# Optimization experiments

Measured on AMD Instinct MI355X. Metric: run time of the kernel, lower is better.

Reference implementation:

```python
import jax, jax.numpy as jnp
import numpy as np

STALK_DIM = 8
K = 5
MARGIN = 0.5
TAU = 0.01
EPS_GAP = 1e-4


def _sheaf_eigenvalues(points, W):
    """Eigenvalues of the sheaf Laplacian L = delta^T delta on a point cloud.

    points: (n, d_in), W: (s, d_in) projection weight (nn.Linear, no bias).
    Faithful to the torch loop, but assembles L directly from its s x s blocks
    (L = delta^T delta expanded per edge) instead of materializing dense delta.
    """
    X = points @ W.T                       # (n, s)
    n, s = X.shape

    # --- fixed topology: KNN on detached coordinates (torch no_grad) ---
    Xd = jax.lax.stop_gradient(X)
    d2 = jnp.sum((Xd[:, None, :] - Xd[None, :, :]) ** 2, axis=-1)  # (n, n)
    nn_idx = jnp.argsort(d2, axis=1)[:, 1:K + 1]                    # (n, K), skip self
    A = jnp.zeros((n, n), dtype=bool).at[jnp.arange(n)[:, None], nn_idx].set(True)
    A = A | A.T                                                     # undirected
    triu = jnp.triu(jnp.ones((n, n), dtype=bool), 1)
    M = (A & triu).astype(points.dtype)    # (n, n) edge mask, canonical i < j

    # --- restriction maps for all ordered pairs i < j (mask selects edges) ---
    d = X[None, :, :] - X[:, None, :]      # d[i, j] = X[j] - X[i], (n, n, s)
    dn = jnp.linalg.norm(d, axis=-1) + 1e-12
    dhat = d / dn[..., None]
    alpha = jnp.minimum(dn, 1.0)
    I_s = jnp.eye(s, dtype=points.dtype)
    # R_ij = I - alpha * dhat dhat^T   (n, n, s, s)
    R = I_s - alpha[..., None, None] * (dhat[..., :, None] * dhat[..., None, :])
    RtR = jnp.einsum('ijab,ijac->ijbc', R, R)

    # --- L = delta^T delta, per edge (i<j): row block [.. I .. -R ..]
    #     contributes  L[i,i]+=I,  L[j,j]+=R^T R,  L[i,j]+=-R,  L[j,i]+=-R^T
    Off = -(M[..., None, None] * R)                     # nonzero only for i<j
    Lb = Off + jnp.swapaxes(jnp.swapaxes(Off, 0, 1), 2, 3)  # add lower blocks
    deg = M.sum(axis=1)                                  # I-blocks at node i
    Djj = jnp.einsum('ij,ijab->jab', M, RtR)             # R^T R blocks at node j
    diag = deg[:, None, None] * I_s + Djj                # (n, s, s)
    Lb = Lb.at[jnp.arange(n), jnp.arange(n)].add(diag)
    L = Lb.transpose(0, 2, 1, 3).reshape(n * s, n * s)
    L = 0.5 * (L + L.T)

    eigs = jnp.linalg.eigvalsh(L)          # ascending, (n*s,)
    return jnp.clip(eigs, 0.0)


def _spectral_gap(eigs):
    gates = jax.nn.sigmoid((eigs - EPS_GAP) / TAU)
    return jnp.sum(eigs * gates) / (jnp.sum(gates) + 1e-12)


def setup_inputs() -> dict:
    key = jax.random.key(0)
    kq, kp, kn, kw = jax.random.split(key, 4)
    n_q, n_pn, d_in = 256, 256, 768
    q_emb = jax.random.normal(kq, (n_q, d_in), dtype=jnp.float32)
    pos_emb = jax.random.normal(kp, (n_pn, d_in), dtype=jnp.float32)
    neg_emb = jax.random.normal(kn, (n_pn, d_in), dtype=jnp.float32)
    # orthogonal init for the projection, as in nn.init.orthogonal_
    G = jax.random.normal(kw, (d_in, STALK_DIM), dtype=jnp.float32)
    Q, _ = jnp.linalg.qr(G)                # (d_in, s) with orthonormal columns
    W = Q.T                                # (s, d_in)
    return {"q_emb": q_emb, "pos_emb": pos_emb, "neg_emb": neg_emb, "W": W}


def reference(q_emb, pos_emb, neg_emb, W):
    pos_cloud = jnp.concatenate([q_emb, pos_emb], axis=0)
    neg_cloud = jnp.concatenate([q_emb, neg_emb], axis=0)
    gap_pos = _spectral_gap(_sheaf_eigenvalues(pos_cloud, W))
    gap_neg = _spectral_gap(_sheaf_eigenvalues(neg_cloud, W))
    triplet = jax.nn.relu(gap_pos - gap_neg + MARGIN)
    return triplet + 0.1 * gap_pos
```

## Files before the change

kernel.cpp:

```cpp
#include <hip/hip_runtime.h>
#include <math.h>

#define NLS    4096
#define NNODE  512
#define SDIM   8
#define KNN_K  5
#define MAXNBR 128
#define DIN    768
#define NB     32
#define GMEGA  448

#define AGLD(p)    __hip_atomic_load((p), __ATOMIC_RELAXED, __HIP_MEMORY_SCOPE_AGENT)
#define AGST(p, v) __hip_atomic_store((p), (v), __ATOMIC_RELAXED, __HIP_MEMORY_SCOPE_AGENT)

struct Ptrs {
  float* X;
  int*   nn;
  int*   nbr;
  int*   cnt;
  float* y;
  float* acol;
  float* vtw;
  float* darr;
  float* ebuf;
  float* e2;
  float* bounds;
  float* eigs;
  float* Vt;
  float* Wt;
  float* c1;
  float* c2;
  int*   barmem;
  float* A0;
  float* A1;
};

__device__ __forceinline__ float* matA(const Ptrs& p, int cloud) {
  return cloud == 0 ? p.A0 : p.A1;
}

__device__ __forceinline__ void tbar(int* bm, int act, int bid, int& gen,
                                     int& leafbase, int& rootbase, bool fence) {
  __syncthreads();
  if (threadIdx.x == 0) {
    gen += 1;
    int perleaf = act >> 5;
    if (fence) __threadfence();
    else       __builtin_amdgcn_s_waitcnt(0);
    int* leaf = bm + ((bid & 31) << 4);
    int old = __hip_atomic_fetch_add(leaf, 1, __ATOMIC_RELAXED, __HIP_MEMORY_SCOPE_AGENT);
    if (old == leafbase + perleaf - 1) {
      int ro = __hip_atomic_fetch_add(bm + 512, 1, __ATOMIC_RELAXED, __HIP_MEMORY_SCOPE_AGENT);
      if (ro == rootbase + 31) AGST(bm + 768, gen);
    }
    leafbase += perleaf;
    rootbase += 32;
    while (AGLD(bm + 768) < gen) __builtin_amdgcn_s_sleep(16);
    if (fence) __threadfence();
  }
  __syncthreads();
}

__global__ void zero_kernel(float* ptr, long n) {
  long i = (long)blockIdx.x * 256 + threadIdx.x;
  if (i < n) ptr[i] = 0.f;
}

__global__ void proj_kernel(Ptrs p, const float* q, const float* pe,
                            const float* ne, const float* W) {
  int idx = blockIdx.x * 256 + threadIdx.x;
  if (idx >= 2 * NNODE * SDIM) return;
  int cloud = idx >> 12;
  int rem   = idx & 4095;
  int node  = rem >> 3, t = rem & 7;
  const float* src = (node < 256) ? (q + (size_t)node * DIN)
                                  : ((cloud == 0 ? pe : ne) + (size_t)(node - 256) * DIN);
  const float* wr = W + (size_t)t * DIN;
  float acc = 0.f;
  for (int i = 0; i < DIN; ++i) acc += src[i] * wr[i];
  p.X[(cloud * NNODE + node) * SDIM + t] = acc;
}

__global__ void knn_kernel(Ptrs p) {
  int i = blockIdx.x, cloud = blockIdx.z;
  int lane = threadIdx.x;
  __shared__ float d2s[NNODE];
  const float* X = p.X + cloud * NNODE * SDIM;
  float xi[SDIM];
  for (int t = 0; t < SDIM; ++t) xi[t] = X[i * SDIM + t];
  for (int j = lane; j < NNODE; j += 64) {
    float s = 0.f;
    for (int t = 0; t < SDIM; ++t) { float d = xi[t] - X[j * SDIM + t]; s += d * d; }
    d2s[j] = (j == i) ? 3.4e38f : s;
  }
  __syncthreads();
  for (int r = 0; r < KNN_K; ++r) {
    float bv = 3.39e38f; int bi = NNODE;
    for (int j = lane; j < NNODE; j += 64) {
      float val = d2s[j];
      if (val < bv || (val == bv && j < bi)) { bv = val; bi = j; }
    }
    for (int o = 32; o > 0; o >>= 1) {
      float ov = __shfl_down(bv, o); int oi = __shfl_down(bi, o);
      if (ov < bv || (ov == bv && oi < bi)) { bv = ov; bi = oi; }
    }
    if (lane == 0) {
      p.nn[(cloud * NNODE + i) * KNN_K + r] = bi;
      d2s[bi] = 3.4e38f;
    }
    __syncthreads();
  }
}

__global__ void adj_kernel(Ptrs p) {
  int idx = blockIdx.x * 256 + threadIdx.x;
  if (idx >= 2 * NNODE) return;
  int cloud = idx >> 9, i = idx & 511;
  const int* nn = p.nn + cloud * NNODE * KNN_K;
  int c = 0;
  for (int j = 0; j < NNODE; ++j) {
    if (j == i) continue;
    bool e = false;
    for (int r = 0; r < KNN_K; ++r)
      if (nn[i * KNN_K + r] == j || nn[j * KNN_K + r] == i) e = true;
    if (e) { if (c < MAXNBR) p.nbr[(cloud * NNODE + i) * MAXNBR + c] = j; ++c; }
  }
  p.cnt[cloud * NNODE + i] = (c > MAXNBR ? MAXNBR : c);
}

__global__ void assemble_kernel(Ptrs p, int cloud0) {
  int i = blockIdx.x;
  int cloud = cloud0 + blockIdx.z;
  float* A = matA(p, cloud);
  const float* X = p.X + cloud * NNODE * SDIM;
  const int* nbr = p.nbr + (cloud * NNODE + i) * MAXNBR;
  int cnt = p.cnt[cloud * NNODE + i];
  int tid = threadIdx.x;

  for (int idx = tid; idx < SDIM * NLS; idx += 256) {
    int t = idx >> 12;
    int c = idx & 4095;
    A[(size_t)(i * SDIM + t) * NLS + c] = 0.f;
  }
  __shared__ float diag[64];
  __shared__ float xi[SDIM];
  if (tid < SDIM) xi[tid] = X[i * SDIM + tid];
  if (tid < 64)   diag[tid] = 0.f;
  __syncthreads();

  for (int s = 0; s < cnt; ++s) {
    int j = nbr[s];
    float d[SDIM], ss = 0.f;
    for (int t = 0; t < SDIM; ++t) { d[t] = X[j * SDIM + t] - xi[t]; ss += d[t] * d[t]; }
    float dn = sqrtf(ss) + 1e-12f;
    float alpha = dn < 1.f ? dn : 1.f;
    float inv = 1.f / dn;
    if (tid < 64) {
      int t = tid >> 3, t2 = tid & 7;
      float ut = d[t] * inv, ut2 = d[t2] * inv;
      A[(size_t)(i * SDIM + t) * NLS + j * SDIM + t2] =
          alpha * ut * ut2 - (t == t2 ? 1.f : 0.f);
      if (j < i) {
        float beta = 2.f * alpha - alpha * alpha;
        diag[tid] += beta * ut * ut2;
      }
    }
  }
  __syncthreads();
  if (tid < 64) {
    int t = tid >> 3, t2 = tid & 7;
    A[(size_t)(i * SDIM + t) * NLS + i * SDIM + t2] =
        (t == t2 ? (float)cnt : 0.f) - diag[tid];
  }
}

__global__ __launch_bounds__(256, 4) void mega_kernel(Ptrs p, int cloud0) {
  const int cloud = cloud0 + blockIdx.z;
  const int bid = blockIdx.x;
  float* A  = matA(p, cloud);
  float* Vt = p.Vt + (size_t)cloud * NB * NLS;
  float* Wt = p.Wt + (size_t)cloud * NB * NLS;
  float* yv = p.y + (size_t)cloud * NLS;
  float* acol = p.acol + (size_t)cloud * NLS;
  float* c1g = p.c1 + (size_t)cloud * NLS * NB;
  float* c2g = p.c2 + (size_t)cloud * NLS * NB;
  int* bm = p.barmem + (size_t)cloud * 2048;
  int gen = 0, leafbase = 0, rootbase = 0;
  const int tid = threadIdx.x, lane = tid & 63, wv = tid >> 6;

  __shared__ union {
    float v[NLS + 4];
    struct { float Vr[NB][64], Wr[NB][64], Vc[NB][64], Wc[NB][64]; } t;
  } sh;
  __shared__ float c1w[4][NB], c2w[4][NB];
  __shared__ float c1s[NB], c2s[NB], vks[NB], wks[NB];
  __shared__ float red4[4];

  for (int k0 = 0; k0 + NB <= NLS - 64; k0 += NB) {
    int act = (NLS - k0) >> 3;
    act = (act + 31) & ~31;
    if (act < 64)    act = 64;
    if (act > GMEGA) act = GMEGA;
    if (bid >= act) return;

    for (int jj = 0; jj < NB; ++jj) {
      const int k = k0 + jj, s = k + 1, m = NLS - s;
      const int vbase = s & ~3, vn = NLS - vbase;
      const float* src = (jj == 0) ? (A + (size_t)k * NLS) : acol;

      float xp = 0.f;
      for (int i = tid; i < vn; i += 256) {
        int c = vbase + i;
        float a = (c < s) ? 0.f : AGLD((float*)&src[c]);
        sh.v[i] = a;
        if (c > s) xp += a * a;
      }
      for (int o = 32; o > 0; o >>= 1) xp += __shfl_down(xp, o);
      if (lane == 0) red4[wv] = xp;
      __syncthreads();
      float xnorm2 = red4[0] + red4[1] + red4[2] + red4[3];
      float alpha = sh.v[s - vbase];
      float tau, scale;
      {
        float beta;
        if (xnorm2 > 0.f) {
          beta  = -copysignf(sqrtf(alpha * alpha + xnorm2), alpha);
          tau   = (beta - alpha) / beta;
          scale = 1.f / (alpha - beta);
        } else { beta = alpha; tau = 0.f; scale = 0.f; }
        if (bid == 0 && tid == 0) {
          p.darr[cloud * NLS + k] = AGLD((float*)&src[k]);
          p.ebuf[cloud * NLS + k] = beta;
        }
      }
      __syncthreads();
      for (int i = tid; i < vn; i += 256) {
        int c = vbase + i;
        sh.v[i] = (c == s) ? 1.f : ((c < s) ? 0.f : sh.v[i] * scale);
      }
      __syncthreads();

      const int nwav = act << 2;
      int B = (m + nwav - 1) / nwav;
      B = (B + 1) & ~1;
      const int r0 = s + ((bid << 2) + wv) * B;
      int r1 = r0 + B; if (r1 > NLS) r1 = NLS;
      float vtyloc = 0.f, c1p = 0.f, c2p = 0.f;
      const int l2i = lane - 32;
      for (int r = r0; r < r1; r += 2) {
        const bool two = (r + 1 < r1);
        const float* Ar0 = A + (size_t)r * NLS;
        const float* Ar1 = two ? (Ar0 + NLS) : Ar0;
        float acc0 = 0.f, acc1 = 0.f;
        #pragma unroll 4
        for (int c = vbase + (lane << 2); c < NLS; c += 256) {
          const float4 v4 = *(const float4*)(&sh.v[c - vbase]);
          const float4 a0 = *(const float4*)(Ar0 + c);
          const float4 a1 = *(const float4*)(Ar1 + c);
          acc0 += a0.x * v4.x + a0.y * v4.y + a0.z * v4.z + a0.w * v4.w;
          acc1 += a1.x * v4.x + a1.y * v4.y + a1.z * v4.z + a1.w * v4.w;
        }
        for (int o = 32; o > 0; o >>= 1) {
          acc0 += __shfl_down(acc0, o);
          acc1 += __shfl_down(acc1, o);
        }
        float vr0 = sh.v[r - vbase];
        float vr1 = two ? sh.v[r + 1 - vbase] : 0.f;
        if (lane == 0) {
          AGST(&yv[r], acc0);
          if (two) AGST(&yv[r + 1], acc1);
          vtyloc += vr0 * acc0 + vr1 * acc1;
        }
        if (lane < jj) {
          const float* Wl = Wt + (size_t)lane * NLS;
          c1p += Wl[r] * vr0 + (two ? Wl[r + 1] * vr1 : 0.f);
        }
        if (l2i >= 0 && l2i < jj) {
          const float* Vl = Vt + (size_t)l2i * NLS;
          c2p += Vl[r] * vr0 + (two ? Vl[r + 1] * vr1 : 0.f);
        }
      }
      if (lane == 0) red4[wv] = vtyloc;
      if (lane < 32)      c1w[wv][lane] = (lane < jj) ? c1p : 0.f;
      else                c2w[wv][l2i]  = (l2i  < jj) ? c2p : 0.f;
      __syncthreads();
      if (tid == 0) {
        float t = red4[0] + red4[1] + red4[2] + red4[3];
        if (t != 0.f) atomicAdd(&p.vtw[cloud * NLS + k], t);
      }
      if (tid < jj) {
        float t = c1w[0][tid] + c1w[1][tid] + c1w[2][tid] + c1w[3][tid];
        if (t != 0.f) atomicAdd(&c1g[(size_t)k * NB + tid], t);
      } else if (tid >= 64 && tid < 64 + jj) {
        int j2 = tid - 64;
        float t = c2w[0][j2] + c2w[1][j2] + c2w[2][j2] + c2w[3][j2];
        if (t != 0.f) atomicAdd(&c2g[(size_t)k * NB + j2], t);
      }

      tbar(bm, act, bid, gen, leafbase, rootbase, false);

      if (tid < jj) {
        c1s[tid] = AGLD(&c1g[(size_t)k * NB + tid]);
        c2s[tid] = AGLD(&c2g[(size_t)k * NB + tid]);
        vks[tid] = Vt[(size_t)tid * NLS + s];
        wks[tid] = Wt[(size_t)tid * NLS + s];
      }
      __syncthreads();
      float vty = AGLD(&p.vtw[cloud * NLS + k]);
      float dotc = 0.f, corrs = 0.f;
      for (int j2 = 0; j2 < jj; ++j2) {
        dotc  += c1s[j2] * c2s[j2];
        corrs += vks[j2] * c1s[j2] + wks[j2] * c2s[j2];
      }
      float s2v = tau * (vty - 2.f * dotc);
      float ys  = AGLD(&yv[s]);
      float wfirst = tau * ys - tau * corrs - 0.5f * tau * s2v;
      bool havenext = (jj < NB - 1);
      const float* Arow = A + (size_t)s * NLS;
      for (int r = s + (bid << 8) + tid; r < NLS; r += (act << 8)) {
        float vr = sh.v[r - vbase];
        float yr = AGLD(&yv[r]);
        float corr = 0.f, ac2 = 0.f;
        for (int j2 = 0; j2 < jj; ++j2) {
          float vj = Vt[(size_t)j2 * NLS + r];
          float wj = Wt[(size_t)j2 * NLS + r];
          corr += vj * c1s[j2] + wj * c2s[j2];
          ac2  += vj * wks[j2] + wj * vks[j2];
        }
        float wr = tau * yr - tau * corr - 0.5f * tau * s2v * vr;
        AGST(&Vt[(size_t)jj * NLS + r], vr);
        AGST(&Wt[(size_t)jj * NLS + r], wr);
        if (havenext) AGST(&acol[r], Arow[r] - ac2 - (vr * wfirst + wr));
      }

      tbar(bm, act, bid, gen, leafbase, rootbase, false);
    }

    {
      const int base2 = k0 + NB;
      const int nt = (NLS - base2 + 63) >> 6;
      const int ntt = nt * nt;
      for (int it = bid; it < ntt; it += act) {
        int by = it / nt, bx = it - by * nt;
        int r0t = base2 + (by << 6), c0t = base2 + (bx << 6);
        __syncthreads();
        for (int idx = tid; idx < NB * 64; idx += 256) {
          int j4 = idx >> 6, i = idx & 63;
          int r = r0t + i, c = c0t + i;
          sh.t.Vr[j4][i] = (r < NLS) ? Vt[(size_t)j4 * NLS + r] : 0.f;
          sh.t.Wr[j4][i] = (r < NLS) ? Wt[(size_t)j4 * NLS + r] : 0.f;
          sh.t.Vc[j4][i] = (c < NLS) ? Vt[(size_t)j4 * NLS + c] : 0.f;
          sh.t.Wc[j4][i] = (c < NLS) ? Wt[(size_t)j4 * NLS + c] : 0.f;
        }
        __syncthreads();
        int ty = tid >> 4, tx = tid & 15;
        float acc[4][4] = {{0.f}};
        for (int j4 = 0; j4 < NB; ++j4) {
          float vr[4], wr[4], vc[4], wc[4];
          for (int a = 0; a < 4; ++a) {
            vr[a] = sh.t.Vr[j4][ty * 4 + a]; wr[a] = sh.t.Wr[j4][ty * 4 + a];
            vc[a] = sh.t.Vc[j4][tx * 4 + a]; wc[a] = sh.t.Wc[j4][tx * 4 + a];
          }
          for (int a = 0; a < 4; ++a)
            for (int b = 0; b < 4; ++b)
              acc[a][b] += vr[a] * wc[b] + wr[a] * vc[b];
        }
        for (int a = 0; a < 4; ++a) {
          int r = r0t + ty * 4 + a;
          int c = c0t + tx * 4;
          if (r < NLS && c < NLS) {
            float4* pa = (float4*)&A[(size_t)r * NLS + c];
            float4 old = *pa;
            old.x -= acc[a][0]; old.y -= acc[a][1];
            old.z -= acc[a][2]; old.w -= acc[a][3];
            *pa = old;
          }
        }
      }
      tbar(bm, act, bid, gen, leafbase, rootbase, true);
    }
  }
}

__global__ void ktrail_kernel(Ptrs p, int cloud0) {
  int cloud = cloud0 + blockIdx.z;
  float* A = matA(p, cloud);
  const int base = NLS - 64;
  int lane = threadIdx.x;
  __shared__ float B[64][65];
  __shared__ float vv[64], ww[64];
  for (int r = 0; r < 64; ++r)
    B[r][lane] = A[(size_t)(base + r) * NLS + base + lane];
  __syncthreads();
  for (int kl = 0; kl <= 61; ++kl) {
    float val = (lane >= kl + 2) ? B[kl][lane] : 0.f;
    float part = val * val;
    for (int o = 32; o > 0; o >>= 1) part += __shfl_xor(part, o);
    float xnorm2 = part;
    float alpha = B[kl][kl + 1];
    float beta, tau, scale;
    if (xnorm2 > 0.f) {
      beta  = -copysignf(sqrtf(alpha * alpha + xnorm2), alpha);
      tau   = (beta - alpha) / beta;
      scale = 1.f / (alpha - beta);
    } else { beta = alpha; tau = 0.f; scale = 0.f; }
    if (lane == 0) {
      p.darr[cloud * NLS + base + kl] = B[kl][kl];
      p.ebuf[cloud * NLS + base + kl] = beta;
    }
    vv[lane] = (lane == kl + 1) ? 1.f : ((lane >= kl + 2) ? B[kl][lane] * scale : 0.f);
    __syncthreads();
    float yv = 0.f;
    if (lane >= kl + 1)
      for (int c = kl + 1; c < 64; ++c) yv += B[lane][c] * vv[c];
    float vy = (lane >= kl + 1) ? vv[lane] * yv : 0.f;
    for (int o = 32; o > 0; o >>= 1) vy += __shfl_xor(vy, o);
    float w = tau * yv - 0.5f * tau * (tau * vy) * vv[lane];
    ww[lane] = (lane >= kl + 1) ? w : 0.f;
    __syncthreads();
    if (lane >= kl + 1) {
      float vr = vv[lane], wr = ww[lane];
      for (int c = kl + 1; c < 64; ++c)
        B[lane][c] -= vr * ww[c] + wr * vv[c];
    }
    __syncthreads();
  }
  if (lane == 0) {
    p.darr[cloud * NLS + base + 62] = B[62][62];
    p.darr[cloud * NLS + base + 63] = B[63][63];
    p.ebuf[cloud * NLS + base + 62] = B[63][62];
    p.ebuf[cloud * NLS + base + 63] = 0.f;
  }
}

__global__ void gather_kernel(Ptrs p, int cloud0) {
  int cloud = cloud0 + blockIdx.z;
  const int n = NLS;
  int tid = threadIdx.x;
  const float* d = p.darr + cloud * NLS;
  float* e2 = p.e2 + cloud * NLS;
  __shared__ float elds[NLS];
  for (int i = tid; i < n; i += 1024) {
    float e = (i < n - 1) ? p.ebuf[cloud * NLS + i] : 0.f;
    e2[i]   = e * e;
    elds[i] = fabsf(e);
  }
  __syncthreads();
  float lo = 3.4e38f, hi = -3.4e38f;
  for (int i = tid; i < n; i += 1024) {
    float rad = elds[i] + (i > 0 ? elds[i - 1] : 0.f);
    lo = fminf(lo, d[i] - rad);
    hi = fmaxf(hi, d[i] + rad);
  }
  __shared__ float rl[16], rh[16];
  int lane = tid & 63, wv = tid >> 6;
  for (int o = 32; o > 0; o >>= 1) {
    lo = fminf(lo, __shfl_down(lo, o));
    hi = fmaxf(hi, __shfl_down(hi, o));
  }
  if (lane == 0) { rl[wv] = lo; rh[wv] = hi; }
  __syncthreads();
  if (tid == 0) {
    for (int t = 1; t < 16; ++t) { lo = fminf(lo, rl[t]); hi = fmaxf(hi, rh[t]); }
    p.bounds[cloud * 2 + 0] = lo - 0.5f;
    p.bounds[cloud * 2 + 1] = hi + 0.5f;
  }
}

__global__ void bisect_kernel(Ptrs p, int cloud0) {
  int cloud = cloud0 + blockIdx.z;
  int idx = blockIdx.x * 256 + threadIdx.x;
  const float* d  = p.darr + cloud * NLS;
  const float* e2 = p.e2   + cloud * NLS;
  float lo = p.bounds[cloud * 2 + 0];
  float hi = p.bounds[cloud * 2 + 1];
  const float pivmin = 1e-28f;
  for (int it = 0; it < 34; ++it) {
    float mid = 0.5f * (lo + hi);
    int cnt = 0;
    float qq = d[0] - mid;
    if (fabsf(qq) < pivmin) qq = -pivmin;
    cnt += (qq < 0.f);
    for (int i = 1; i < NLS; ++i) {
      qq = d[i] - mid - e2[i - 1] / qq;
      if (fabsf(qq) < pivmin) qq = -pivmin;
      cnt += (qq < 0.f);
    }
    if (cnt > idx) hi = mid; else lo = mid;
  }
  float ev = 0.5f * (lo + hi);
  p.eigs[cloud * NLS + idx] = ev > 0.f ? ev : 0.f;
}

__global__ void final_kernel(Ptrs p, float* out) {
  __shared__ float lds[64];
  int tid = threadIdx.x;
  for (int cloud = 0; cloud < 2; ++cloud) {
    float num = 0.f, den = 0.f;
    for (int i = tid; i < NLS; i += 256) {
      float lam = p.eigs[cloud * NLS + i];
      float g = 1.f / (1.f + expf(-(lam - 1e-4f) * 100.f));
      num += lam * g;
      den += g;
    }
    for (int o = 32; o > 0; o >>= 1) {
      num += __shfl_down(num, o);
      den += __shfl_down(den, o);
    }
    if ((tid & 63) == 0) { lds[(tid >> 6) * 2] = num; lds[(tid >> 6) * 2 + 1] = den; }
    __syncthreads();
    if (tid == 0) {
      float N = lds[0] + lds[2] + lds[4] + lds[6];
      float D = lds[1] + lds[3] + lds[5] + lds[7];
      lds[32 + cloud] = N / (D + 1e-12f);
    }
    __syncthreads();
  }
  if (tid == 0) {
    float gp = lds[32], gn = lds[33];
    float trip = gp - gn + 0.5f;
    if (trip < 0.f) trip = 0.f;
    out[0] = trip + 0.1f * gp;
  }
}

extern "C" void kernel_launch(void* const* d_in, const int* in_sizes, int n_in,
                              void* d_out, int out_size, void* d_ws, size_t ws_size,
                              hipStream_t stream) {
  const float* q  = (const float*)d_in[0];
  const float* pe = (const float*)d_in[1];
  const float* ne = (const float*)d_in[2];
  const float* W  = (const float*)d_in[3];

  char* base = (char*)d_ws;
  size_t off = 0;
  auto alloc = [&](size_t nbytes) -> void* {
    off = (off + 255) & ~(size_t)255;
    void* r = base + off;
    off += nbytes;
    return r;
  };

  Ptrs p;
  p.X      = (float*)alloc(sizeof(float) * 2 * NNODE * SDIM);
  p.nn     = (int*)  alloc(sizeof(int)   * 2 * NNODE * KNN_K);
  p.nbr    = (int*)  alloc(sizeof(int)   * 2 * NNODE * MAXNBR);
  p.cnt    = (int*)  alloc(sizeof(int)   * 2 * NNODE);
  p.y      = (float*)alloc(sizeof(float) * 2 * NLS);
  p.acol   = (float*)alloc(sizeof(float) * 2 * NLS);
  p.darr   = (float*)alloc(sizeof(float) * 2 * NLS);
  p.ebuf   = (float*)alloc(sizeof(float) * 2 * NLS);
  p.e2     = (float*)alloc(sizeof(float) * 2 * NLS);
  p.bounds = (float*)alloc(sizeof(float) * 4);
  p.eigs   = (float*)alloc(sizeof(float) * 2 * NLS);
  p.Vt     = (float*)alloc(sizeof(float) * 2 * NB * NLS);
  p.Wt     = (float*)alloc(sizeof(float) * 2 * NB * NLS);

  size_t zstart = (off + 255) & ~(size_t)255;
  p.vtw    = (float*)alloc(sizeof(float) * 2 * NLS);
  p.c1     = (float*)alloc(sizeof(float) * 2 * NLS * NB);
  p.c2     = (float*)alloc(sizeof(float) * 2 * NLS * NB);
  p.barmem = (int*)  alloc(sizeof(int)   * 2 * 2048);
  size_t zend = off;
  long zcount = (long)((zend - zstart) / 4);

  const size_t Abytes = (size_t)NLS * NLS * sizeof(float);
  p.A0 = (float*)alloc(Abytes);
  size_t offA1 = (off + 255) & ~(size_t)255;
  bool batched = (offA1 + Abytes) <= ws_size;
  p.A1 = batched ? (float*)alloc(Abytes) : p.A0;

  zero_kernel<<<dim3((int)((zcount + 255) / 256)), 256, 0, stream>>>((float*)(base + zstart), zcount);
  proj_kernel<<<dim3(32), 256, 0, stream>>>(p, q, pe, ne, W);
  knn_kernel<<<dim3(NNODE, 1, 2), 64, 0, stream>>>(p);
  adj_kernel<<<dim3(4), 256, 0, stream>>>(p);

  auto run_cloud = [&](int cloud0, int z) {
    assemble_kernel<<<dim3(NNODE, 1, z), 256, 0, stream>>>(p, cloud0);
    mega_kernel<<<dim3(GMEGA, 1, z), 256, 0, stream>>>(p, cloud0);
    ktrail_kernel<<<dim3(1, 1, z), 64, 0, stream>>>(p, cloud0);
    gather_kernel<<<dim3(1, 1, z), 1024, 0, stream>>>(p, cloud0);
    bisect_kernel<<<dim3(NLS / 256, 1, z), 256, 0, stream>>>(p, cloud0);
  };

  if (batched) {
    run_cloud(0, 2);
  } else {
    run_cloud(0, 1);
    run_cloud(1, 1);
  }

  final_kernel<<<dim3(1), 256, 0, stream>>>(p, (float*)d_out);
}
```

Before: 107.4 ms.

## Fuse Householder norm into column update and raise persistent grid occupancy

Each block now accumulates the squared norm of the next Householder column while writing acol and adds it atomically into a zeroed xn2 buffer. Later columns can then compute beta, tau and scale straight away, which removes one block-wide reduction and one __syncthreads per column. The trailing-update tile now loads V/W in two halves of 16 to shrink shared memory. Launch bounds rise to 6 blocks per CU, the grid cap rises to 640 and the active-block heuristic changes. The matvec loop is also unrolled with split accumulators. The risks are more grid-barrier participants and a changed floating-point summation order for the norm.

```diff
diff --git a/kernel.cpp b/kernel.cpp
--- a/kernel.cpp
+++ b/kernel.cpp
@@ -8,7 +8,7 @@
 #define MAXNBR 128
 #define DIN    768
 #define NB     32
-#define GMEGA  448
+#define GMEGA  640
 
 #define AGLD(p)    __hip_atomic_load((p), __ATOMIC_RELAXED, __HIP_MEMORY_SCOPE_AGENT)
 #define AGST(p, v) __hip_atomic_store((p), (v), __ATOMIC_RELAXED, __HIP_MEMORY_SCOPE_AGENT)
@@ -21,6 +21,7 @@
   float* y;
   float* acol;
   float* vtw;
+  float* xn2;
   float* darr;
   float* ebuf;
   float* e2;
@@ -174,7 +175,7 @@
   }
 }
 
-__global__ __launch_bounds__(256, 4) void mega_kernel(Ptrs p, int cloud0) {
+__global__ __launch_bounds__(256, 6) void mega_kernel(Ptrs p, int cloud0) {
   const int cloud = cloud0 + blockIdx.z;
   const int bid = blockIdx.x;
   float* A  = matA(p, cloud);
@@ -184,20 +185,21 @@
   float* acol = p.acol + (size_t)cloud * NLS;
   float* c1g = p.c1 + (size_t)cloud * NLS * NB;
   float* c2g = p.c2 + (size_t)cloud * NLS * NB;
+  float* xn2g = p.xn2 + (size_t)cloud * NLS;
   int* bm = p.barmem + (size_t)cloud * 2048;
   int gen = 0, leafbase = 0, rootbase = 0;
   const int tid = threadIdx.x, lane = tid & 63, wv = tid >> 6;
 
-  __shared__ union {
+  __shared__ __align__(16) union {
     float v[NLS + 4];
-    struct { float Vr[NB][64], Wr[NB][64], Vc[NB][64], Wc[NB][64]; } t;
+    struct { float Vr[16][64], Wr[16][64], Vc[16][64], Wc[16][64]; } t;
   } sh;
   __shared__ float c1w[4][NB], c2w[4][NB];
   __shared__ float c1s[NB], c2s[NB], vks[NB], wks[NB];
   __shared__ float red4[4];
 
   for (int k0 = 0; k0 + NB <= NLS - 64; k0 += NB) {
-    int act = (NLS - k0) >> 3;
+    int act = (NLS - k0) / 6;
     act = (act + 31) & ~31;
     if (act < 64)    act = 64;
     if (act > GMEGA) act = GMEGA;
@@ -206,22 +208,22 @@
     for (int jj = 0; jj < NB; ++jj) {
       const int k = k0 + jj, s = k + 1, m = NLS - s;
       const int vbase = s & ~3, vn = NLS - vbase;
-      const float* src = (jj == 0) ? (A + (size_t)k * NLS) : acol;
-
-      float xp = 0.f;
-      for (int i = tid; i < vn; i += 256) {
-        int c = vbase + i;
-        float a = (c < s) ? 0.f : AGLD((float*)&src[c]);
-        sh.v[i] = a;
-        if (c > s) xp += a * a;
-      }
-      for (int o = 32; o > 0; o >>= 1) xp += __shfl_down(xp, o);
-      if (lane == 0) red4[wv] = xp;
-      __syncthreads();
-      float xnorm2 = red4[0] + red4[1] + red4[2] + red4[3];
-      float alpha = sh.v[s - vbase];
+
       float tau, scale;
-      {
+      if (jj == 0) {
+        const float* src = A + (size_t)k * NLS;
+        float xp = 0.f;
+        for (int i = tid; i < vn; i += 256) {
+          int c = vbase + i;
+          float a = (c < s) ? 0.f : AGLD((float*)&src[c]);
+          sh.v[i] = a;
+          if (c > s) xp += a * a;
+        }
+        for (int o = 32; o > 0; o >>= 1) xp += __shfl_down(xp, o);
+        if (lane == 0) red4[wv] = xp;
+        __syncthreads();
+        float xnorm2 = red4[0] + red4[1] + red4[2] + red4[3];
+        float alpha = sh.v[s - vbase];
         float beta;
         if (xnorm2 > 0.f) {
           beta  = -copysignf(sqrtf(alpha * alpha + xnorm2), alpha);
@@ -232,13 +234,32 @@
           p.darr[cloud * NLS + k] = AGLD((float*)&src[k]);
           p.ebuf[cloud * NLS + k] = beta;
         }
-      }
-      __syncthreads();
-      for (int i = tid; i < vn; i += 256) {
-        int c = vbase + i;
-        sh.v[i] = (c == s) ? 1.f : ((c < s) ? 0.f : sh.v[i] * scale);
-      }
-      __syncthreads();
+        __syncthreads();
+        for (int i = tid; i < vn; i += 256) {
+          int c = vbase + i;
+          sh.v[i] = (c == s) ? 1.f : ((c < s) ? 0.f : sh.v[i] * scale);
+        }
+        __syncthreads();
+      } else {
+        float xnorm2 = AGLD(&xn2g[k]);
+        float alpha  = AGLD(&acol[s]);
+        float beta;
+        if (xnorm2 > 0.f) {
+          beta  = -copysignf(sqrtf(alpha * alpha + xnorm2), alpha);
+          tau   = (beta - alpha) / beta;
+          scale = 1.f / (alpha - beta);
+        } else { beta = alpha; tau = 0.f; scale = 0.f; }
+        if (bid == 0 && tid == 0) {
+          p.darr[cloud * NLS + k] = AGLD(&acol[k]);
+          p.ebuf[cloud * NLS + k] = beta;
+        }
+        for (int i = tid; i < vn; i += 256) {
+          int c = vbase + i;
+          float a = (c < s) ? 0.f : AGLD(&acol[c]);
+          sh.v[i] = (c == s) ? 1.f : a * scale;
+        }
+        __syncthreads();
+      }
 
       const int nwav = act << 2;
       int B = (m + nwav - 1) / nwav;
@@ -251,15 +272,29 @@
         const bool two = (r + 1 < r1);
         const float* Ar0 = A + (size_t)r * NLS;
         const float* Ar1 = two ? (Ar0 + NLS) : Ar0;
-        float acc0 = 0.f, acc1 = 0.f;
-        #pragma unroll 4
-        for (int c = vbase + (lane << 2); c < NLS; c += 256) {
-          const float4 v4 = *(const float4*)(&sh.v[c - vbase]);
-          const float4 a0 = *(const float4*)(Ar0 + c);
-          const float4 a1 = *(const float4*)(Ar1 + c);
-          acc0 += a0.x * v4.x + a0.y * v4.y + a0.z * v4.z + a0.w * v4.w;
-          acc1 += a1.x * v4.x + a1.y * v4.y + a1.z * v4.z + a1.w * v4.w;
-        }
+        float a0e = 0.f, a0o = 0.f, a1e = 0.f, a1o = 0.f;
+        int c = vbase + (lane << 2);
+        #pragma unroll 2
+        for (; c + 260 <= NLS; c += 512) {
+          const float4 ve = *(const float4*)(&sh.v[c - vbase]);
+          const float4 vo = *(const float4*)(&sh.v[c + 256 - vbase]);
+          const float4 x0e = *(const float4*)(Ar0 + c);
+          const float4 x0o = *(const float4*)(Ar0 + c + 256);
+          const float4 x1e = *(const float4*)(Ar1 + c);
+          const float4 x1o = *(const float4*)(Ar1 + c + 256);
+          a0e += x0e.x * ve.x + x0e.y * ve.y + x0e.z * ve.z + x0e.w * ve.w;
+          a0o += x0o.x * vo.x + x0o.y * vo.y + x0o.z * vo.z + x0o.w * vo.w;
+          a1e += x1e.x * ve.x + x1e.y * ve.y + x1e.z * ve.z + x1e.w * ve.w;
+          a1o += x1o.x * vo.x + x1o.y * vo.y + x1o.z * vo.z + x1o.w * vo.w;
+        }
+        if (c < NLS) {
+          const float4 ve = *(const float4*)(&sh.v[c - vbase]);
+          const float4 x0e = *(const float4*)(Ar0 + c);
+          const float4 x1e = *(const float4*)(Ar1 + c);
+          a0e += x0e.x * ve.x + x0e.y * ve.y + x0e.z * ve.z + x0e.w * ve.w;
+          a1e += x1e.x * ve.x + x1e.y * ve.y + x1e.z * ve.z + x1e.w * ve.w;
+        }
+        float acc0 = a0e + a0o, acc1 = a1e + a1o;
         for (int o = 32; o > 0; o >>= 1) {
           acc0 += __shfl_down(acc0, o);
           acc1 += __shfl_down(acc1, o);
@@ -317,6 +352,7 @@
       float wfirst = tau * ys - tau * corrs - 0.5f * tau * s2v;
       bool havenext = (jj < NB - 1);
       const float* Arow = A + (size_t)s * NLS;
+      float xpart = 0.f;
       for (int r = s + (bid << 8) + tid; r < NLS; r += (act << 8)) {
         float vr = sh.v[r - vbase];
         float yr = AGLD(&yv[r]);
@@ -330,7 +366,20 @@
         float wr = tau * yr - tau * corr - 0.5f * tau * s2v * vr;
         AGST(&Vt[(size_t)jj * NLS + r], vr);
         AGST(&Wt[(size_t)jj * NLS + r], wr);
-        if (havenext) AGST(&acol[r], Arow[r] - ac2 - (vr * wfirst + wr));
+        if (havenext) {
+          float ac = Arow[r] - ac2 - (vr * wfirst + wr);
+          AGST(&acol[r], ac);
+          if (r >= s + 2) xpart += ac * ac;
+        }
+      }
+      if (havenext) {
+        for (int o = 32; o > 0; o >>= 1) xpart += __shfl_down(xpart, o);
+        if (lane == 0) red4[wv] = xpart;
+        __syncthreads();
+        if (tid == 0) {
+          float t = red4[0] + red4[1] + red4[2] + red4[3];
+          if (t != 0.f) atomicAdd(&xn2g[k + 1], t);
+        }
       }
 
       tbar(bm, act, bid, gen, leafbase, rootbase, false);
@@ -343,27 +392,30 @@
       for (int it = bid; it < ntt; it += act) {
         int by = it / nt, bx = it - by * nt;
         int r0t = base2 + (by << 6), c0t = base2 + (bx << 6);
-        __syncthreads();
-        for (int idx = tid; idx < NB * 64; idx += 256) {
-          int j4 = idx >> 6, i = idx & 63;
-          int r = r0t + i, c = c0t + i;
-          sh.t.Vr[j4][i] = (r < NLS) ? Vt[(size_t)j4 * NLS + r] : 0.f;
-          sh.t.Wr[j4][i] = (r < NLS) ? Wt[(size_t)j4 * NLS + r] : 0.f;
-          sh.t.Vc[j4][i] = (c < NLS) ? Vt[(size_t)j4 * NLS + c] : 0.f;
-          sh.t.Wc[j4][i] = (c < NLS) ? Wt[(size_t)j4 * NLS + c] : 0.f;
-        }
-        __syncthreads();
         int ty = tid >> 4, tx = tid & 15;
         float acc[4][4] = {{0.f}};
-        for (int j4 = 0; j4 < NB; ++j4) {
-          float vr[4], wr[4], vc[4], wc[4];
-          for (int a = 0; a < 4; ++a) {
-            vr[a] = sh.t.Vr[j4][ty * 4 + a]; wr[a] = sh.t.Wr[j4][ty * 4 + a];
-            vc[a] = sh.t.Vc[j4][tx * 4 + a]; wc[a] = sh.t.Wc[j4][tx * 4 + a];
+        for (int half = 0; half < 2; ++half) {
+          __syncthreads();
+          for (int idx = tid; idx < 16 * 64; idx += 256) {
+            int j4 = idx >> 6, i = idx & 63;
+            int jg = (half << 4) + j4;
+            int r = r0t + i, c = c0t + i;
+            sh.t.Vr[j4][i] = (r < NLS) ? Vt[(size_t)jg * NLS + r] : 0.f;
+            sh.t.Wr[j4][i] = (r < NLS) ? Wt[(size_t)jg * NLS + r] : 0.f;
+            sh.t.Vc[j4][i] = (c < NLS) ? Vt[(size_t)jg * NLS + c] : 0.f;
+            sh.t.Wc[j4][i] = (c < NLS) ? Wt[(size_t)jg * NLS + c] : 0.f;
           }
-          for (int a = 0; a < 4; ++a)
-            for (int b = 0; b < 4; ++b)
-              acc[a][b] += vr[a] * wc[b] + wr[a] * vc[b];
+          __syncthreads();
+          for (int j4 = 0; j4 < 16; ++j4) {
+            float vr[4], wr[4], vc[4], wc[4];
+            for (int a = 0; a < 4; ++a) {
+              vr[a] = sh.t.Vr[j4][ty * 4 + a]; wr[a] = sh.t.Wr[j4][ty * 4 + a];
+              vc[a] = sh.t.Vc[j4][tx * 4 + a]; wc[a] = sh.t.Wc[j4][tx * 4 + a];
+            }
+            for (int a = 0; a < 4; ++a)
+              for (int b = 0; b < 4; ++b)
+                acc[a][b] += vr[a] * wc[b] + wr[a] * vc[b];
+          }
         }
         for (int a = 0; a < 4; ++a) {
           int r = r0t + ty * 4 + a;
@@ -558,6 +610,7 @@
 
   size_t zstart = (off + 255) & ~(size_t)255;
   p.vtw    = (float*)alloc(sizeof(float) * 2 * NLS);
+  p.xn2    = (float*)alloc(sizeof(float) * 2 * NLS);
   p.c1     = (float*)alloc(sizeof(float) * 2 * NLS * NB);
   p.c2     = (float*)alloc(sizeof(float) * 2 * NLS * NB);
   p.barmem = (int*)  alloc(sizeof(int)   * 2 * 2048);
```

Result: slower. 232.9 ms (+116.9%).
